# Optimization experiments

Hardware: AMD Instinct MI355X
Metric: run time of the kernel (lower is better)

The kernel has to match this reference:

```python
import jax, jax.numpy as jnp
import numpy as np

B, T, N = 64, 256, 8192
D_EMB, D_ATT = 32, 128


def setup_inputs() -> dict:
    keys = iter(jax.random.split(jax.random.key(0), 64))
    nk = lambda: next(keys)
    inp = {}
    inp["x_ped"] = jax.random.normal(nk(), (B, T, 4), jnp.float32)
    inp["x_ego"] = jax.random.normal(nk(), (B, T, 4), jnp.float32)
    inp["h_ped"] = jax.random.normal(nk(), (B, D_EMB), jnp.float32)
    dims = {"neighbor": 4, "light": 6, "sign": 5, "crosswalk": 7, "station": 7}
    for name, d in dims.items():
        inp["x_" + name] = jax.random.normal(nk(), (N, T, d), jnp.float32)
        # class labels; -1 marks invalid/padded object at that timestep
        inp["cls_" + name] = jax.random.randint(nk(), (N, T), -1, 3, dtype=jnp.int32)
        inp["seg_" + name] = jnp.sort(jax.random.randint(nk(), (N,), 0, B, dtype=jnp.int32))

    def lin(din, dout):
        k1, k2 = jax.random.split(nk())
        return (jax.random.normal(k1, (din, dout), jnp.float32) / float(np.sqrt(din)),
                jax.random.normal(k2, (dout,), jnp.float32) * 0.01)

    inp["Wp"], inp["bp"] = lin(4, D_EMB)      # target_box_embedding
    inp["Wn"], inp["bn"] = lin(4, D_EMB)      # x_neighbor embedding
    inp["Wl"], inp["bl"] = lin(6, D_EMB)      # x_light
    inp["Wsi"], inp["bsi"] = lin(5, D_EMB)    # x_sign
    inp["Wc"], inp["bc"] = lin(7, D_EMB)      # x_crosswalk
    inp["Wst"], inp["bst"] = lin(7, D_EMB)    # x_station
    inp["We"], inp["be"] = lin(4, D_EMB)      # x_ego
    inp["Wax"], _ = lin(D_EMB, D_ATT)         # additive attention: value proj
    inp["Wah"], inp["ba"] = lin(D_EMB, D_ATT)  # additive attention: query proj
    inp["va"] = jax.random.normal(nk(), (D_ATT,), jnp.float32) / float(np.sqrt(D_ATT))
    inp["W1"], inp["b1"] = lin(7 * D_EMB, D_EMB)  # classifier (6 traffic types + ped)
    inp["W2"], inp["b2"] = lin(D_EMB, D_EMB)
    inp["W3"], inp["b3"] = lin(D_EMB, 1)
    inp["t"] = 8
    return inp


def _masked_segment_softmax(score, mask, seg, num_segments):
    # equals torch.exp(score)/segment_sum(exp) over valid objects, stably
    s = jnp.where(mask, score, -1e30)
    smax = jax.ops.segment_max(s, seg, num_segments=num_segments)
    smax = jnp.where(smax > -1e29, smax, 0.0)  # empty segments -> 0
    e = jnp.where(mask, jnp.exp(score - smax[seg]), 0.0)
    denom = jax.ops.segment_sum(e, seg, num_segments=num_segments)
    return e / jnp.maximum(denom[seg], 1e-30)


def _attend_type(x, cls, seg, W, b, h_ped, Wax, Wah, ba, va, t):
    emb_t = jax.nn.relu(x[:, t] @ W + b)                    # [N, 32]
    mask = cls[:, t] != -1                                   # [N]
    # additive attention score: v^T tanh(Wx*x + Wh*h + b)
    score = jnp.tanh(emb_t @ Wax + h_ped[seg] @ Wah + ba) @ va  # [N]
    probs = _masked_segment_softmax(score, mask, seg, B)     # [N], 0 where masked
    # identity-matmul scatter-add in the original == segment_sum
    feat = jax.ops.segment_sum(emb_t * probs[:, None], seg, num_segments=B)  # [B, 32]
    return feat, probs


def reference(x_ped, x_ego, h_ped,
              x_neighbor, cls_neighbor, seg_neighbor,
              x_light, cls_light, seg_light,
              x_sign, cls_sign, seg_sign,
              x_crosswalk, cls_crosswalk, seg_crosswalk,
              x_station, cls_station, seg_station,
              Wp, bp, Wn, bn, Wl, bl, Wsi, bsi, Wc, bc, Wst, bst, We, be,
              Wax, Wah, ba, va, W1, b1, W2, b2, W3, b3, t):
    ped_t = jax.nn.relu(x_ped[:, t] @ Wp + bp)               # [B, 32]
    ego_t = jax.nn.relu(x_ego[:, t] @ We + be)               # ego is a plain tensor (cls_ego is Tensor)
    f_n, p_n = _attend_type(x_neighbor, cls_neighbor, seg_neighbor, Wn, bn, h_ped, Wax, Wah, ba, va, t)
    f_l, p_l = _attend_type(x_light, cls_light, seg_light, Wl, bl, h_ped, Wax, Wah, ba, va, t)
    f_si, p_si = _attend_type(x_sign, cls_sign, seg_sign, Wsi, bsi, h_ped, Wax, Wah, ba, va, t)
    f_c, p_c = _attend_type(x_crosswalk, cls_crosswalk, seg_crosswalk, Wc, bc, h_ped, Wax, Wah, ba, va, t)
    f_st, p_st = _attend_type(x_station, cls_station, seg_station, Wst, bst, h_ped, Wax, Wah, ba, va, t)
    feats = jnp.concatenate([ped_t, f_n, f_l, f_si, f_c, f_st, ego_t], axis=-1)  # [B, 224]
    # classifier (dropout is identity in eval)
    h1 = jax.nn.relu(feats @ W1 + b1)
    h2 = jax.nn.relu(h1 @ W2 + b2)
    int_det_score = h2 @ W3 + b3                             # [B, 1]
    return int_det_score, feats, p_n, p_l, p_si, p_c, p_st
```

## Files before the change

### kernel.cpp

```cpp
#include <hip/hip_runtime.h>

#define TSTEPS 256
#define NOBJ   8192
#define BATCH  64
#define DEMB   32
#define DATT   128

#define HW_OFF     0
#define EX_OFF     32768
#define SEGOFF_OFF 196608
#define EMB_OFF    199168
#define WS_NEED    (EMB_OFF + 5 * NOBJ * DEMB * 4)

struct SP {
    const float* x[5]; const int* cls[5]; const int* seg[5];
    const float* W[5]; const float* bias[5];
    const float* x_ped; const float* x_ego; const float* h_ped;
    const float* Wp; const float* bp; const float* We; const float* be;
    const float* Wax; const float* Wah; const float* ba; const float* va;
    const float* W1; const float* b1; const float* W2; const float* b2;
    const float* W3; const float* b3;
    const int* t_ptr;
    float* out;
    float* hW;
    float* ex;
    int* seg_off;
    float* emb;
    int d[5];
    int use_emb;
};

__device__ __forceinline__ int load_t(const void* p) {
    unsigned w0 = *(const unsigned*)p;
    if (w0 < (unsigned)TSTEPS) return (int)w0;
    float f = __uint_as_float(w0);
    if (f >= 0.f && f < 256.f) return (int)f;
    return 8;
}

__device__ __forceinline__ float fast_tanh(float x) {
    float e = __expf(2.0f * x);
    return 1.0f - 2.0f / (e + 1.0f);
}

__device__ __forceinline__ int lower_bound(const int* a, int n, int v) {
    int lo = 0, hi = n;
    while (lo < hi) { int mid = (lo + hi) >> 1; if (a[mid] < v) lo = mid + 1; else hi = mid; }
    return lo;
}

__global__ __launch_bounds__(128) void k_prep(SP p) {
    const int b = blockIdx.x;
    const int j = threadIdx.x;
    const int t = load_t(p.t_ptr);
    float a = p.ba[j];
    const float* h = p.h_ped + b * DEMB;
    #pragma unroll
    for (int k = 0; k < DEMB; ++k) a += h[k] * p.Wah[k * DATT + j];
    p.hW[b * DATT + j] = a;

    if (j < DEMB) {
        const float* xp = p.x_ped + (size_t)(b * TSTEPS + t) * 4;
        float e = p.bp[j];
        #pragma unroll
        for (int k = 0; k < 4; ++k) e += xp[k] * p.Wp[k * DEMB + j];
        p.out[64 + b * 224 + j] = fmaxf(e, 0.f);
        const float* xe = p.x_ego + (size_t)(b * TSTEPS + t) * 4;
        float g = p.be[j];
        #pragma unroll
        for (int k = 0; k < 4; ++k) g += xe[k] * p.We[k * DEMB + j];
        p.out[64 + b * 224 + 192 + j] = fmaxf(g, 0.f);
    }
    if (j < 5) p.seg_off[j * 65 + b] = lower_bound(p.seg[j], NOBJ, b);
    if (b == 63 && j >= 5 && j < 10) p.seg_off[(j - 5) * 65 + 64] = NOBJ;
}

template<int D>
__device__ __forceinline__ void score_body(const SP& p, const int type, const int t,
                                           float* WaxT, float* W_s, float* b_s) {
    const int tid = threadIdx.x;
    const float* __restrict__ x   = p.x[type];
    const int*   __restrict__ cls = p.cls[type];
    const int*   __restrict__ seg = p.seg[type];

    const int q = tid & 15;
    const int o = tid >> 4;
    const int i0 = blockIdx.x * 32 + o;
    const int i1 = i0 + 16;

    const int c0 = cls[i0 * TSTEPS + t];
    const int c1 = cls[i1 * TSTEPS + t];
    const int b0 = seg[i0];
    const int b1 = seg[i1];
    float xv0[D], xv1[D];
    {
        const float* xr0 = x + (size_t)(i0 * TSTEPS + t) * D;
        const float* xr1 = x + (size_t)(i1 * TSTEPS + t) * D;
        #pragma unroll
        for (int k = 0; k < D; ++k) { xv0[k] = xr0[k]; xv1[k] = xr1[k]; }
    }

    for (int i = tid; i < DATT * DEMB; i += 256) {
        const int j = i >> 5, k = i & 31;
        WaxT[i] = p.Wax[k * DATT + j];
    }
    for (int i = tid; i < D * DEMB; i += 256) W_s[i] = p.W[type][i];
    if (tid < DEMB) b_s[tid] = p.bias[type][tid];
    __syncthreads();

    float e0[DEMB], e1[DEMB];
    const float4* b4 = (const float4*)b_s;
    #pragma unroll
    for (int cc = 0; cc < 8; ++cc) {
        const int c = (cc + q) & 7;
        float4 a0 = b4[c], a1 = b4[c];
        #pragma unroll
        for (int k = 0; k < D; ++k) {
            const float4 w = *(const float4*)&W_s[k * DEMB + 4 * c];
            a0.x += xv0[k]*w.x; a0.y += xv0[k]*w.y; a0.z += xv0[k]*w.z; a0.w += xv0[k]*w.w;
            a1.x += xv1[k]*w.x; a1.y += xv1[k]*w.y; a1.z += xv1[k]*w.z; a1.w += xv1[k]*w.w;
        }
        e0[4*cc+0]=fmaxf(a0.x,0.f); e0[4*cc+1]=fmaxf(a0.y,0.f);
        e0[4*cc+2]=fmaxf(a0.z,0.f); e0[4*cc+3]=fmaxf(a0.w,0.f);
        e1[4*cc+0]=fmaxf(a1.x,0.f); e1[4*cc+1]=fmaxf(a1.y,0.f);
        e1[4*cc+2]=fmaxf(a1.z,0.f); e1[4*cc+3]=fmaxf(a1.w,0.f);
    }

    float hv0[8], hv1[8], vv[8];
    {
        const float* hp0 = p.hW + b0 * DATT + q * 8;
        const float* hp1 = p.hW + b1 * DATT + q * 8;
        const float* vp  = p.va + q * 8;
        *(float4*)(hv0)   = *(const float4*)(hp0);
        *(float4*)(hv0+4) = *(const float4*)(hp0+4);
        *(float4*)(hv1)   = *(const float4*)(hp1);
        *(float4*)(hv1+4) = *(const float4*)(hp1+4);
        *(float4*)(vv)    = *(const float4*)(vp);
        *(float4*)(vv+4)  = *(const float4*)(vp+4);
    }

    float sc0 = 0.f, sc1 = 0.f;
    #pragma unroll
    for (int jo = 0; jo < 8; ++jo) {
        const float* wrow = &WaxT[(q * 8 + jo) * DEMB];
        float s0a=0.f, s0b=0.f, s1a=0.f, s1b=0.f;
        #pragma unroll
        for (int cc = 0; cc < 8; ++cc) {
            const int c = (cc + q) & 7;
            const float4 w = *(const float4*)&wrow[4 * c];
            s0a += e0[4*cc+0]*w.x + e0[4*cc+1]*w.y;
            s0b += e0[4*cc+2]*w.z + e0[4*cc+3]*w.w;
            s1a += e1[4*cc+0]*w.x + e1[4*cc+1]*w.y;
            s1b += e1[4*cc+2]*w.z + e1[4*cc+3]*w.w;
        }
        sc0 += fast_tanh(hv0[jo] + (s0a + s0b)) * vv[jo];
        sc1 += fast_tanh(hv1[jo] + (s1a + s1b)) * vv[jo];
    }
    sc0 += __shfl_xor(sc0, 1); sc1 += __shfl_xor(sc1, 1);
    sc0 += __shfl_xor(sc0, 2); sc1 += __shfl_xor(sc1, 2);
    sc0 += __shfl_xor(sc0, 4); sc1 += __shfl_xor(sc1, 4);
    sc0 += __shfl_xor(sc0, 8); sc1 += __shfl_xor(sc1, 8);

    if (q == 0) {
        p.ex[type * NOBJ + i0] = (c0 != -1) ? __expf(sc0) : 0.f;
        p.ex[type * NOBJ + i1] = (c1 != -1) ? __expf(sc1) : 0.f;
    }
    if (p.use_emb && q < 8) {
        *(float4*)&p.emb[((size_t)type * NOBJ + i0) * DEMB + 4 * q] = make_float4(e0[0],e0[1],e0[2],e0[3]);
        *(float4*)&p.emb[((size_t)type * NOBJ + i1) * DEMB + 4 * q] = make_float4(e1[0],e1[1],e1[2],e1[3]);
    }
}

__global__ __launch_bounds__(256, 4) void k_score(SP p) {
    __shared__ __align__(16) float WaxT[DATT * DEMB];
    __shared__ __align__(16) float W_s[7 * DEMB];
    __shared__ __align__(16) float b_s[DEMB];
    const int t = load_t(p.t_ptr);
    switch (blockIdx.y) {
        case 0: score_body<4>(p, 0, t, WaxT, W_s, b_s); break;
        case 1: score_body<6>(p, 1, t, WaxT, W_s, b_s); break;
        case 2: score_body<5>(p, 2, t, WaxT, W_s, b_s); break;
        case 3: score_body<7>(p, 3, t, WaxT, W_s, b_s); break;
        default: score_body<7>(p, 4, t, WaxT, W_s, b_s); break;
    }
}

__global__ __launch_bounds__(256) void k_finish(SP p) {
    const int type = blockIdx.y;
    const int bseg = blockIdx.x;
    const int tid  = threadIdx.x;
    const int j    = tid & 31;
    const int sl   = tid >> 5;
    const int wv   = tid >> 6;
    const float* __restrict__ ex = p.ex + type * NOBJ;
    const int lo = p.seg_off[type * 65 + bseg];
    const int hi = p.seg_off[type * 65 + bseg + 1];

    __shared__ float red4[4];
    __shared__ float ared[4][DEMB];

    float s = 0.f;
    for (int i = lo + tid; i < hi; i += 256) s += ex[i];
    #pragma unroll
    for (int off = 32; off; off >>= 1) s += __shfl_xor(s, off);
    if ((tid & 63) == 0) red4[wv] = s;
    __syncthreads();
    const float inv = 1.0f / fmaxf(red4[0] + red4[1] + red4[2] + red4[3], 1e-30f);

    float acc = 0.f;
    float* pout = p.out + 64 + BATCH * 224 + type * NOBJ;
    if (p.use_emb) {
        const float* __restrict__ eb = p.emb + (size_t)type * NOBJ * DEMB;
        for (int i = lo + sl; i < hi; i += 8) {
            const float pr = ex[i] * inv;
            if (j == 0) pout[i] = pr;
            acc += pr * eb[(size_t)i * DEMB + j];
        }
    } else {
        const int t = load_t(p.t_ptr);
        const int d = p.d[type];
        float wj[7];
        for (int k = 0; k < d; ++k) wj[k] = p.W[type][k * DEMB + j];
        const float bj = p.bias[type][j];
        for (int i = lo + sl; i < hi; i += 8) {
            const float e = ex[i];
            const float pr = e * inv;
            if (j == 0) pout[i] = pr;
            if (e > 0.f) {
                const float* xr = p.x[type] + (size_t)(i * TSTEPS + t) * d;
                float a = bj;
                for (int k = 0; k < d; ++k) a += xr[k] * wj[k];
                acc += pr * fmaxf(a, 0.f);
            }
        }
    }
    acc += __shfl_xor(acc, 32);
    if ((tid & 63) < 32) ared[wv][j] = acc;
    __syncthreads();
    if (tid < DEMB) {
        const float f = ared[0][tid] + ared[1][tid] + ared[2][tid] + ared[3][tid];
        p.out[64 + bseg * 224 + 32 * (1 + type) + tid] = f;
    }
}

__global__ __launch_bounds__(64) void k_head(SP p) {
    const int b   = blockIdx.x;
    const int tid = threadIdx.x;
    const int j    = tid & 31;
    const int half = tid >> 5;
    __shared__ float h1s[DEMB];
    __shared__ float h2s[DEMB];
    const float* feats = p.out + 64 + b * 224;

    float a = 0.f;
    const int k0 = half * 112;
    #pragma unroll 4
    for (int k = k0; k < k0 + 112; ++k)
        a += feats[k] * p.W1[k * DEMB + j];
    a += __shfl_xor(a, 32);
    if (half == 0) h1s[j] = fmaxf(a + p.b1[j], 0.f);
    __syncthreads();

    float a2 = 0.f;
    const int k2 = half * 16;
    #pragma unroll
    for (int k = k2; k < k2 + 16; ++k)
        a2 += h1s[k] * p.W2[k * DEMB + j];
    a2 += __shfl_xor(a2, 32);
    if (half == 0) h2s[j] = fmaxf(a2 + p.b2[j], 0.f);
    __syncthreads();

    if (half == 0) {
        float v = h2s[j] * p.W3[j];
        v += __shfl_xor(v, 16); v += __shfl_xor(v, 8);
        v += __shfl_xor(v, 4);  v += __shfl_xor(v, 2); v += __shfl_xor(v, 1);
        if (j == 0) p.out[b] = v + p.b3[0];
    }
}

extern "C" void kernel_launch(void* const* d_in, const int* in_sizes, int n_in,
                              void* d_out, int out_size, void* d_ws, size_t ws_size,
                              hipStream_t stream) {
    (void)in_sizes; (void)n_in; (void)out_size;

    SP p;
    const int xi[5] = {3, 6, 9, 12, 15};
    const int wi[5] = {20, 22, 24, 26, 28};
    const int di[5] = {4, 6, 5, 7, 7};
    for (int tp = 0; tp < 5; ++tp) {
        p.x[tp]    = (const float*)d_in[xi[tp]];
        p.cls[tp]  = (const int*)d_in[xi[tp] + 1];
        p.seg[tp]  = (const int*)d_in[xi[tp] + 2];
        p.W[tp]    = (const float*)d_in[wi[tp]];
        p.bias[tp] = (const float*)d_in[wi[tp] + 1];
        p.d[tp]    = di[tp];
    }
    p.x_ped = (const float*)d_in[0];
    p.x_ego = (const float*)d_in[1];
    p.h_ped = (const float*)d_in[2];
    p.Wp = (const float*)d_in[18]; p.bp = (const float*)d_in[19];
    p.We = (const float*)d_in[30]; p.be = (const float*)d_in[31];
    p.Wax = (const float*)d_in[32]; p.Wah = (const float*)d_in[33];
    p.ba  = (const float*)d_in[34]; p.va  = (const float*)d_in[35];
    p.W1 = (const float*)d_in[36]; p.b1 = (const float*)d_in[37];
    p.W2 = (const float*)d_in[38]; p.b2 = (const float*)d_in[39];
    p.W3 = (const float*)d_in[40]; p.b3 = (const float*)d_in[41];
    p.t_ptr = (const int*)d_in[42];
    p.out = (float*)d_out;
    char* ws = (char*)d_ws;
    p.hW      = (float*)(ws + HW_OFF);
    p.ex      = (float*)(ws + EX_OFF);
    p.seg_off = (int*)(ws + SEGOFF_OFF);
    p.emb     = (float*)(ws + EMB_OFF);
    p.use_emb = (ws_size >= (size_t)WS_NEED) ? 1 : 0;

    hipLaunchKernelGGL(k_prep,   dim3(BATCH),         dim3(DATT), 0, stream, p);
    hipLaunchKernelGGL(k_score,  dim3(NOBJ / 32, 5),  dim3(256),  0, stream, p);
    hipLaunchKernelGGL(k_finish, dim3(BATCH, 5),      dim3(256),  0, stream, p);
    hipLaunchKernelGGL(k_head,   dim3(BATCH),         dim3(64),   0, stream, p);
}
```

Before: 51.00 us.

## Fuse embedding and attention projection loops; compute segment offsets from boundaries

The score kernel now folds each 4-wide chunk of the ReLU embedding straight into eight per-thread attention accumulators. This removes the two 32-element embedding arrays held in registers, and the embedding store moves inside that loop. The occupancy hint of 4 blocks per unit is dropped, and the hW/va loads move ahead of the shared-memory fill. Segment offsets are now built by extra prep blocks that detect boundaries in the sorted segment arrays, replacing per-batch binary searches. The intent is less register pressure in the score kernel and less serialized prep work, at the cost of a larger prep grid and a redundant scalar store.

New measurement: 44.78 us. -12.2%, faster.

```diff
diff --git a/kernel.cpp b/kernel.cpp
--- a/kernel.cpp
+++ b/kernel.cpp
@@ -43,13 +43,19 @@
     return 1.0f - 2.0f / (e + 1.0f);
 }
 
-__device__ __forceinline__ int lower_bound(const int* a, int n, int v) {
-    int lo = 0, hi = n;
-    while (lo < hi) { int mid = (lo + hi) >> 1; if (a[mid] < v) lo = mid + 1; else hi = mid; }
-    return lo;
-}
-
 __global__ __launch_bounds__(128) void k_prep(SP p) {
+    if (blockIdx.x >= BATCH) {
+        const int g    = (blockIdx.x - BATCH) * 128 + threadIdx.x;
+        const int type = g >> 13;
+        const int i    = g & (NOBJ - 1);
+        const int* __restrict__ seg = p.seg[type];
+        const int sv = seg[i];
+        const int pv = (i == 0) ? -1 : seg[i - 1];
+        for (int v = pv + 1; v <= sv; ++v) p.seg_off[type * 65 + v] = i;
+        if (i == NOBJ - 1)
+            for (int v = sv + 1; v <= BATCH; ++v) p.seg_off[type * 65 + v] = NOBJ;
+        return;
+    }
     const int b = blockIdx.x;
     const int j = threadIdx.x;
     const int t = load_t(p.t_ptr);
@@ -71,8 +77,6 @@
         for (int k = 0; k < 4; ++k) g += xe[k] * p.We[k * DEMB + j];
         p.out[64 + b * 224 + 192 + j] = fmaxf(g, 0.f);
     }
-    if (j < 5) p.seg_off[j * 65 + b] = lower_bound(p.seg[j], NOBJ, b);
-    if (b == 63 && j >= 5 && j < 10) p.seg_off[(j - 5) * 65 + 64] = NOBJ;
 }
 
 template<int D>
@@ -99,33 +103,6 @@
         #pragma unroll
         for (int k = 0; k < D; ++k) { xv0[k] = xr0[k]; xv1[k] = xr1[k]; }
     }
-
-    for (int i = tid; i < DATT * DEMB; i += 256) {
-        const int j = i >> 5, k = i & 31;
-        WaxT[i] = p.Wax[k * DATT + j];
-    }
-    for (int i = tid; i < D * DEMB; i += 256) W_s[i] = p.W[type][i];
-    if (tid < DEMB) b_s[tid] = p.bias[type][tid];
-    __syncthreads();
-
-    float e0[DEMB], e1[DEMB];
-    const float4* b4 = (const float4*)b_s;
-    #pragma unroll
-    for (int cc = 0; cc < 8; ++cc) {
-        const int c = (cc + q) & 7;
-        float4 a0 = b4[c], a1 = b4[c];
-        #pragma unroll
-        for (int k = 0; k < D; ++k) {
-            const float4 w = *(const float4*)&W_s[k * DEMB + 4 * c];
-            a0.x += xv0[k]*w.x; a0.y += xv0[k]*w.y; a0.z += xv0[k]*w.z; a0.w += xv0[k]*w.w;
-            a1.x += xv1[k]*w.x; a1.y += xv1[k]*w.y; a1.z += xv1[k]*w.z; a1.w += xv1[k]*w.w;
-        }
-        e0[4*cc+0]=fmaxf(a0.x,0.f); e0[4*cc+1]=fmaxf(a0.y,0.f);
-        e0[4*cc+2]=fmaxf(a0.z,0.f); e0[4*cc+3]=fmaxf(a0.w,0.f);
-        e1[4*cc+0]=fmaxf(a1.x,0.f); e1[4*cc+1]=fmaxf(a1.y,0.f);
-        e1[4*cc+2]=fmaxf(a1.z,0.f); e1[4*cc+3]=fmaxf(a1.w,0.f);
-    }
-
     float hv0[8], hv1[8], vv[8];
     {
         const float* hp0 = p.hW + b0 * DATT + q * 8;
@@ -139,22 +116,52 @@
         *(float4*)(vv+4)  = *(const float4*)(vp+4);
     }
 
+    for (int i = tid; i < DATT * DEMB; i += 256) {
+        const int j = i >> 5, k = i & 31;
+        WaxT[i] = p.Wax[k * DATT + j];
+    }
+    for (int i = tid; i < D * DEMB; i += 256) W_s[i] = p.W[type][i];
+    if (tid < DEMB) b_s[tid] = p.bias[type][tid];
+    __syncthreads();
+
+    float acc0[8], acc1[8];
+    #pragma unroll
+    for (int jo = 0; jo < 8; ++jo) { acc0[jo] = 0.f; acc1[jo] = 0.f; }
+
+    const float4* b4 = (const float4*)b_s;
+    #pragma unroll
+    for (int cc = 0; cc < 8; ++cc) {
+        const int c = (cc + q) & 7;
+        float4 a0 = b4[c], a1 = b4[c];
+        #pragma unroll
+        for (int k = 0; k < D; ++k) {
+            const float4 w = *(const float4*)&W_s[k * DEMB + 4 * c];
+            a0.x += xv0[k]*w.x; a0.y += xv0[k]*w.y; a0.z += xv0[k]*w.z; a0.w += xv0[k]*w.w;
+            a1.x += xv1[k]*w.x; a1.y += xv1[k]*w.y; a1.z += xv1[k]*w.z; a1.w += xv1[k]*w.w;
+        }
+        a0.x = fmaxf(a0.x, 0.f); a0.y = fmaxf(a0.y, 0.f);
+        a0.z = fmaxf(a0.z, 0.f); a0.w = fmaxf(a0.w, 0.f);
+        a1.x = fmaxf(a1.x, 0.f); a1.y = fmaxf(a1.y, 0.f);
+        a1.z = fmaxf(a1.z, 0.f); a1.w = fmaxf(a1.w, 0.f);
+
+        if (p.use_emb && cc == 0 && q < 8) {
+            p.emb[((size_t)type * NOBJ + i0) * DEMB + 4 * q + 0] = a0.x;
+            *(float4*)&p.emb[((size_t)type * NOBJ + i0) * DEMB + 4 * q] = a0;
+            *(float4*)&p.emb[((size_t)type * NOBJ + i1) * DEMB + 4 * q] = a1;
+        }
+        #pragma unroll
+        for (int jo = 0; jo < 8; ++jo) {
+            const float4 w = *(const float4*)&WaxT[(q * 8 + jo) * DEMB + 4 * c];
+            acc0[jo] += a0.x*w.x + a0.y*w.y + a0.z*w.z + a0.w*w.w;
+            acc1[jo] += a1.x*w.x + a1.y*w.y + a1.z*w.z + a1.w*w.w;
+        }
+    }
+
     float sc0 = 0.f, sc1 = 0.f;
     #pragma unroll
     for (int jo = 0; jo < 8; ++jo) {
-        const float* wrow = &WaxT[(q * 8 + jo) * DEMB];
-        float s0a=0.f, s0b=0.f, s1a=0.f, s1b=0.f;
-        #pragma unroll
-        for (int cc = 0; cc < 8; ++cc) {
-            const int c = (cc + q) & 7;
-            const float4 w = *(const float4*)&wrow[4 * c];
-            s0a += e0[4*cc+0]*w.x + e0[4*cc+1]*w.y;
-            s0b += e0[4*cc+2]*w.z + e0[4*cc+3]*w.w;
-            s1a += e1[4*cc+0]*w.x + e1[4*cc+1]*w.y;
-            s1b += e1[4*cc+2]*w.z + e1[4*cc+3]*w.w;
-        }
-        sc0 += fast_tanh(hv0[jo] + (s0a + s0b)) * vv[jo];
-        sc1 += fast_tanh(hv1[jo] + (s1a + s1b)) * vv[jo];
+        sc0 += fast_tanh(hv0[jo] + acc0[jo]) * vv[jo];
+        sc1 += fast_tanh(hv1[jo] + acc1[jo]) * vv[jo];
     }
     sc0 += __shfl_xor(sc0, 1); sc1 += __shfl_xor(sc1, 1);
     sc0 += __shfl_xor(sc0, 2); sc1 += __shfl_xor(sc1, 2);
@@ -165,13 +172,9 @@
         p.ex[type * NOBJ + i0] = (c0 != -1) ? __expf(sc0) : 0.f;
         p.ex[type * NOBJ + i1] = (c1 != -1) ? __expf(sc1) : 0.f;
     }
-    if (p.use_emb && q < 8) {
-        *(float4*)&p.emb[((size_t)type * NOBJ + i0) * DEMB + 4 * q] = make_float4(e0[0],e0[1],e0[2],e0[3]);
-        *(float4*)&p.emb[((size_t)type * NOBJ + i1) * DEMB + 4 * q] = make_float4(e1[0],e1[1],e1[2],e1[3]);
-    }
-}
-
-__global__ __launch_bounds__(256, 4) void k_score(SP p) {
+}
+
+__global__ __launch_bounds__(256) void k_score(SP p) {
     __shared__ __align__(16) float WaxT[DATT * DEMB];
     __shared__ __align__(16) float W_s[7 * DEMB];
     __shared__ __align__(16) float b_s[DEMB];
@@ -314,8 +317,8 @@
     p.emb     = (float*)(ws + EMB_OFF);
     p.use_emb = (ws_size >= (size_t)WS_NEED) ? 1 : 0;
 
-    hipLaunchKernelGGL(k_prep,   dim3(BATCH),         dim3(DATT), 0, stream, p);
-    hipLaunchKernelGGL(k_score,  dim3(NOBJ / 32, 5),  dim3(256),  0, stream, p);
-    hipLaunchKernelGGL(k_finish, dim3(BATCH, 5),      dim3(256),  0, stream, p);
-    hipLaunchKernelGGL(k_head,   dim3(BATCH),         dim3(64),   0, stream, p);
-}
+    hipLaunchKernelGGL(k_prep,   dim3(BATCH + 5 * NOBJ / 128), dim3(128), 0, stream, p);
+    hipLaunchKernelGGL(k_score,  dim3(NOBJ / 32, 5),           dim3(256), 0, stream, p);
+    hipLaunchKernelGGL(k_finish, dim3(BATCH, 5),               dim3(256), 0, stream, p);
+    hipLaunchKernelGGL(k_head,   dim3(BATCH),                  dim3(64),  0, stream, p);
+}
```
